# Kernel tuning notes

Measured on AMD Instinct MI355X. Metric: run time of the kernel, lower is better.

Reference implementation:

```python
import jax, jax.numpy as jnp
import numpy as np

S = 4096          # seq_len (longformer-large-4096)
H = 1024          # hidden_size
FF = 3072         # ffnn_size (hardcoded)
G = 100           # number of gold mentions
MAX_SPAN = 30     # max_span_length
TOP_LAMBDA = 0.2
LN_EPS = 1e-5
MASK_VAL = 10000.0


def setup_inputs() -> dict:
    key = jax.random.key(0)
    ks = jax.random.split(key, 16)
    sc = 0.02
    sequence_output = jax.random.normal(ks[0], (1, S, H), jnp.float32)
    attention_mask = jnp.ones((1, S), jnp.int32)
    # valid gold spans: 1 <= start <= end < start + MAX_SPAN (so torch's >0 filter keeps all)
    gs = jax.random.randint(ks[1], (G,), 1, S - MAX_SPAN)
    gl = jax.random.randint(ks[2], (G,), 0, MAX_SPAN)
    gold_mentions = jnp.stack([gs, gs + gl], axis=1).astype(jnp.int32)  # [G, 2]
    inp = {
        'sequence_output': sequence_output,
        'attention_mask': attention_mask,
        'gold_mentions': gold_mentions,
        # start_mention_mlp
        'W_sm': jax.random.normal(ks[3], (H, FF), jnp.float32) * sc,
        'b_sm': jnp.zeros((FF,), jnp.float32),
        'g_sm': jnp.ones((FF,), jnp.float32),
        'beta_sm': jnp.zeros((FF,), jnp.float32),
        # end_mention_mlp
        'W_em': jax.random.normal(ks[4], (H, FF), jnp.float32) * sc,
        'b_em': jnp.zeros((FF,), jnp.float32),
        'g_em': jnp.ones((FF,), jnp.float32),
        'beta_em': jnp.zeros((FF,), jnp.float32),
        # classifiers
        'w_start': jax.random.normal(ks[5], (FF,), jnp.float32) * sc,
        'b_start': jnp.zeros((), jnp.float32),
        'w_end': jax.random.normal(ks[6], (FF,), jnp.float32) * sc,
        'b_end': jnp.zeros((), jnp.float32),
        'W_s2e': jax.random.normal(ks[7], (FF, FF), jnp.float32) * sc,
        'b_s2e': jnp.zeros((FF,), jnp.float32),
    }
    return inp


def _fcl(x, W, b, g, beta):
    # dense -> gelu (exact) -> layernorm (dropout is identity in eval)
    h = jax.nn.gelu(x @ W + b, approximate=False)
    mu = jnp.mean(h, axis=-1, keepdims=True)
    var = jnp.mean(jnp.square(h - mu), axis=-1, keepdims=True)
    return (h - mu) * jax.lax.rsqrt(var + LN_EPS) * g + beta


def _forward(sequence_output, attention_mask, gold_mentions,
             W_sm, b_sm, g_sm, beta_sm, W_em, b_em, g_em, beta_em,
             w_start, b_start, w_end, b_end, W_s2e, b_s2e):
    start_reps = _fcl(sequence_output, W_sm, b_sm, g_sm, beta_sm)  # [1,S,FF]
    end_reps = _fcl(sequence_output, W_em, b_em, g_em, beta_em)    # [1,S,FF]

    start_logits = jnp.einsum('bsf,f->bs', start_reps, w_start) + b_start  # [1,S]
    end_logits = jnp.einsum('bsf,f->bs', end_reps, w_end) + b_end          # [1,S]
    temp = start_reps @ W_s2e + b_s2e                                      # [1,S,FF]
    joint = jnp.einsum('bsf,btf->bst', temp, end_reps)                     # [1,S,S]
    mention_logits = joint + start_logits[:, :, None] + end_logits[:, None, :]

    # span mask: start <= end < start + MAX_SPAN (triu(0) then tril(MAX_SPAN-1))
    i = jnp.arange(S)
    mention_mask = ((i[:, None] <= i[None, :]) & (i[None, :] < i[:, None] + MAX_SPAN)
                    ).astype(jnp.float32)[None]  # [1,S,S]
    mention_logits = jnp.clip(mention_logits + (1.0 - mention_mask) * (-MASK_VAL),
                              -MASK_VAL, MASK_VAL)

    # top-k pruning; attention_mask is full so k is static: int(S * 0.2)
    max_k = int(S * TOP_LAMBDA)  # 819
    _, topk_1d = jax.lax.top_k(mention_logits.reshape(1, -1), max_k)  # [1,max_k]
    sorted_idx = jnp.sort(topk_1d, axis=-1)
    topk_start_ids = sorted_idx // S
    topk_end_ids = sorted_idx % S
    span_mask = jnp.ones((1, max_k), jnp.float32)

    # losses
    probs = jax.nn.sigmoid(mention_logits)  # [1,S,S]
    gstart = gold_mentions[:, 0]
    gend = gold_mentions[:, 1]
    gold_probs = probs[0, gstart, gend]
    # torch BCE clamps log at -100
    cost_gold = -jnp.mean(jnp.maximum(jnp.log(gold_probs), -100.0))
    junk = probs.at[0, gstart, gend].set(0.0)
    log1mp = jnp.maximum(jnp.log(1.0 - junk), -100.0)
    cost_junk = -jnp.sum(jnp.where(mention_mask == 1.0, log1mp, 0.0)) / jnp.sum(mention_mask)
    cost_is_mention = (cost_gold + cost_junk)[None]  # [1]

    return topk_start_ids, topk_end_ids, span_mask, sequence_output, cost_is_mention


def reference(sequence_output, attention_mask, gold_mentions,
              W_sm, b_sm, g_sm, beta_sm, W_em, b_em, g_em, beta_em,
              w_start, b_start, w_end, b_end, W_s2e, b_s2e):
    return _forward(sequence_output, attention_mask, gold_mentions,
                    W_sm, b_sm, g_sm, beta_sm, W_em, b_em, g_em, beta_em,
                    w_start, b_start, w_end, b_end, W_s2e, b_s2e)
```

## Files before the change

### kernel.cpp

```cpp
#include <hip/hip_runtime.h>
#include <math.h>

#define S 4096
#define H 1024
#define FF 3072
#define G 100
#define MAXSPAN 30
#define MAXK 819
#define NBAND (S * MAXSPAN)
#define BAND_COUNT 122445.0

#define O_START 0
#define O_END   819
#define O_MASK  1638
#define O_SEQ   2457
#define O_COST  (2457 + S * H)

typedef __bf16 bf16x8 __attribute__((ext_vector_type(8)));
typedef float f32x4 __attribute__((ext_vector_type(4)));
typedef float f32x16 __attribute__((ext_vector_type(16)));


__device__ __forceinline__ float block_reduce_256(float x, volatile float* red) {
  #pragma unroll
  for (int off = 32; off > 0; off >>= 1) x += __shfl_down(x, off, 64);
  int wid = threadIdx.x >> 6;
  int lane = threadIdx.x & 63;
  __syncthreads();
  if (lane == 0) red[wid] = x;
  __syncthreads();
  return red[0] + red[1] + red[2] + red[3];
}

__device__ __forceinline__ unsigned f2key(float f) {
  unsigned b = __float_as_uint(f);
  return (b & 0x80000000u) ? ~b : (b | 0x80000000u);
}

__device__ __forceinline__ unsigned short bf16_rne(float x) {
  unsigned u = __float_as_uint(x);
  unsigned r = ((u >> 16) & 1u) + 0x7FFFu;
  return (unsigned short)((u + r) >> 16);
}

__device__ __forceinline__ void split2(float x, unsigned short& h, unsigned short& l) {
  h = bf16_rne(x);
  float hf = __uint_as_float(((unsigned)h) << 16);
  l = bf16_rne(x - hf);
}

__device__ __forceinline__ void gld16(const void* g, void* l) {
  __builtin_amdgcn_global_load_lds(
      (const __attribute__((address_space(1))) unsigned int*)g,
      (__attribute__((address_space(3))) unsigned int*)l, 16, 0, 0);
}


__global__ __launch_bounds__(256) void pack_a_kernel(const float* __restrict__ A,
                                                     unsigned short* __restrict__ hi,
                                                     unsigned short* __restrict__ lo,
                                                     int K) {
  __shared__ float tile[32][33];
  const int t = threadIdx.x;
  const int tx = t & 31, ty8 = t >> 5;
  const int k0 = blockIdx.x * 32, r0 = blockIdx.y * 32;
  #pragma unroll
  for (int r = ty8; r < 32; r += 8)
    tile[r][tx] = A[(size_t)(r0 + r) * K + k0 + tx];
  __syncthreads();
  if (t < 128) {
    const int kql = t >> 5;
    const int rl = t & 31;
    unsigned short h8[8], l8[8];
    #pragma unroll
    for (int s = 0; s < 8; s++) split2(tile[rl][kql * 8 + s], h8[s], l8[s]);
    const size_t panel = (size_t)(r0 >> 7);
    const int rloc = (r0 & 127) + rl;
    const size_t off = panel * (size_t)(128 * K) + (size_t)(k0 / 8 + kql) * 1024 + (size_t)rloc * 8;
    *(uint4*)(hi + off) = *(const uint4*)h8;
    *(uint4*)(lo + off) = *(const uint4*)l8;
  }
}

__global__ __launch_bounds__(256) void pack_ln_a_kernel(const float* __restrict__ A,
                                                        const float* __restrict__ mu,
                                                        const float* __restrict__ rstd,
                                                        const float* __restrict__ g,
                                                        const float* __restrict__ beta,
                                                        unsigned short* __restrict__ hi,
                                                        unsigned short* __restrict__ lo,
                                                        int K) {
  __shared__ float tile[32][33];
  const int t = threadIdx.x;
  const int tx = t & 31, ty8 = t >> 5;
  const int k0 = blockIdx.x * 32, r0 = blockIdx.y * 32;
  #pragma unroll
  for (int r = ty8; r < 32; r += 8)
    tile[r][tx] = A[(size_t)(r0 + r) * K + k0 + tx];
  __syncthreads();
  if (t < 128) {
    const int kql = t >> 5;
    const int rl = t & 31;
    const int row = r0 + rl;
    const float m = mu[row], rs = rstd[row];
    float4 g0 = *(const float4*)(g + k0 + kql * 8);
    float4 g1 = *(const float4*)(g + k0 + kql * 8 + 4);
    float4 b0 = *(const float4*)(beta + k0 + kql * 8);
    float4 b1 = *(const float4*)(beta + k0 + kql * 8 + 4);
    float gv[8] = {g0.x, g0.y, g0.z, g0.w, g1.x, g1.y, g1.z, g1.w};
    float bv[8] = {b0.x, b0.y, b0.z, b0.w, b1.x, b1.y, b1.z, b1.w};
    unsigned short h8[8], l8[8];
    #pragma unroll
    for (int s = 0; s < 8; s++) {
      float v = (tile[rl][kql * 8 + s] - m) * rs * gv[s] + bv[s];
      split2(v, h8[s], l8[s]);
    }
    const size_t panel = (size_t)(r0 >> 7);
    const int rloc = (r0 & 127) + rl;
    const size_t off = panel * (size_t)(128 * K) + (size_t)(k0 / 8 + kql) * 1024 + (size_t)rloc * 8;
    *(uint4*)(hi + off) = *(const uint4*)h8;
    *(uint4*)(lo + off) = *(const uint4*)l8;
  }
}

__global__ __launch_bounds__(256) void pack_bt_kernel(const float* __restrict__ W,
                                                      unsigned short* __restrict__ hi,
                                                      unsigned short* __restrict__ lo,
                                                      int K, int N) {
  __shared__ float tile[32][33];
  const int t = threadIdx.x;
  const int tx = t & 31, ty8 = t >> 5;
  const int k0 = blockIdx.x * 32, n0 = blockIdx.y * 32;
  #pragma unroll
  for (int r = ty8; r < 32; r += 8)
    tile[r][tx] = W[(size_t)(k0 + r) * N + n0 + tx];
  __syncthreads();
  if (t < 128) {
    const int kql = t >> 5;
    const int nl = t & 31;
    unsigned short h8[8], l8[8];
    #pragma unroll
    for (int s = 0; s < 8; s++) split2(tile[kql * 8 + s][nl], h8[s], l8[s]);
    const size_t panel = (size_t)(n0 >> 7);
    const int nloc = (n0 & 127) + nl;
    const size_t off = panel * (size_t)(128 * K) + (size_t)(k0 / 8 + kql) * 1024 + (size_t)nloc * 8;
    *(uint4*)(hi + off) = *(const uint4*)h8;
    *(uint4*)(lo + off) = *(const uint4*)l8;
  }
}


template <int EPI>
__device__ __forceinline__ void gemm_body(const char* cAh, const char* cAl,
                                          const char* cBh, const char* cBl,
                                          const float* __restrict__ bias,
                                          float* __restrict__ C,
                                          int bm, int bn, int N, int K,
                                          char* smem) {
  const int tid = threadIdx.x;
  const int lane = tid & 63;
  const int wid = __builtin_amdgcn_readfirstlane(tid >> 6);
  const int wm = wid >> 1, wn = wid & 1;
  const int lb = lane * 16;
  const int ldsq = wid * 2048;

  const int khalf = lane >> 5;
  const int r31 = lane & 31;
  const int abase = khalf * 2048 + (wm * 64 + r31) * 16;
  const int bbase = khalf * 2048 + (wn * 64 + r31) * 16;

  f32x16 acc[2][2];
  #pragma unroll
  for (int a = 0; a < 2; a++)
    #pragma unroll
    for (int b = 0; b < 2; b++)
      #pragma unroll
      for (int r = 0; r < 16; r++) acc[a][b][r] = 0.0f;

  for (int k0 = 0; k0 < K; k0 += 32) {
    const size_t qb = (size_t)((k0 >> 3) + wid) * 2048 + lb;
    __syncthreads();
    gld16(cAh + qb,        smem +     0 + ldsq);
    gld16(cAh + qb + 1024, smem +     0 + ldsq + 1024);
    gld16(cAl + qb,        smem +  8192 + ldsq);
    gld16(cAl + qb + 1024, smem +  8192 + ldsq + 1024);
    gld16(cBh + qb,        smem + 16384 + ldsq);
    gld16(cBh + qb + 1024, smem + 16384 + ldsq + 1024);
    gld16(cBl + qb,        smem + 24576 + ldsq);
    gld16(cBl + qb + 1024, smem + 24576 + ldsq + 1024);
    __syncthreads();

    bf16x8 ah[2][2], al[2][2], bh[2][2], bl[2][2];
    #pragma unroll
    for (int ks = 0; ks < 2; ks++) {
      #pragma unroll
      for (int mt = 0; mt < 2; mt++) {
        ah[ks][mt] = *(const bf16x8*)(smem +     0 + ks * 4096 + abase + mt * 512);
        al[ks][mt] = *(const bf16x8*)(smem +  8192 + ks * 4096 + abase + mt * 512);
      }
      #pragma unroll
      for (int nt = 0; nt < 2; nt++) {
        bh[ks][nt] = *(const bf16x8*)(smem + 16384 + ks * 4096 + bbase + nt * 512);
        bl[ks][nt] = *(const bf16x8*)(smem + 24576 + ks * 4096 + bbase + nt * 512);
      }
    }
    #pragma unroll
    for (int ks = 0; ks < 2; ks++)
      #pragma unroll
      for (int mt = 0; mt < 2; mt++)
        #pragma unroll
        for (int nt = 0; nt < 2; nt++) {
          acc[mt][nt] = __builtin_amdgcn_mfma_f32_32x32x16_bf16(ah[ks][mt], bh[ks][nt], acc[mt][nt], 0, 0, 0);
          acc[mt][nt] = __builtin_amdgcn_mfma_f32_32x32x16_bf16(al[ks][mt], bh[ks][nt], acc[mt][nt], 0, 0, 0);
          acc[mt][nt] = __builtin_amdgcn_mfma_f32_32x32x16_bf16(ah[ks][mt], bl[ks][nt], acc[mt][nt], 0, 0, 0);
        }
  }

  #pragma unroll
  for (int mt = 0; mt < 2; mt++) {
    #pragma unroll
    for (int nt = 0; nt < 2; nt++) {
      const int colg = bn + wn * 64 + nt * 32 + r31;
      const float bb = bias[colg];
      #pragma unroll
      for (int reg = 0; reg < 16; reg++) {
        const int rowl = (reg & 3) + 8 * (reg >> 2) + 4 * khalf;
        const int rowg = bm + wm * 64 + mt * 32 + rowl;
        float v = acc[mt][nt][reg] + bb;
        if (EPI == 1) v = 0.5f * v * (1.0f + erff(v * 0.70710678118654752f));
        C[(size_t)rowg * N + colg] = v;
      }
    }
  }
}

__global__ __launch_bounds__(256) void gemm_mfma_kernel(const unsigned short* __restrict__ Ahi,
                                                        const unsigned short* __restrict__ Alo,
                                                        const unsigned short* __restrict__ Bhi,
                                                        const unsigned short* __restrict__ Blo,
                                                        const float* __restrict__ bias,
                                                        float* __restrict__ C,
                                                        int N, int K) {
  __shared__ __align__(16) char smem[32768];
  const size_t panAb = (size_t)blockIdx.y * (size_t)(128 * K) * 2;
  const size_t panBb = (size_t)blockIdx.x * (size_t)(128 * K) * 2;
  gemm_body<0>((const char*)Ahi + panAb, (const char*)Alo + panAb,
               (const char*)Bhi + panBb, (const char*)Blo + panBb,
               bias, C, blockIdx.y * 128, blockIdx.x * 128, N, K, smem);
}

__global__ __launch_bounds__(256) void gemm_mfma_dual_kernel(const unsigned short* __restrict__ Ahi,
                                                             const unsigned short* __restrict__ Alo,
                                                             const unsigned short* __restrict__ B1hi,
                                                             const unsigned short* __restrict__ B1lo,
                                                             const unsigned short* __restrict__ B2hi,
                                                             const unsigned short* __restrict__ B2lo,
                                                             const float* __restrict__ bias1,
                                                             const float* __restrict__ bias2,
                                                             float* __restrict__ C1,
                                                             float* __restrict__ C2,
                                                             int N, int K) {
  __shared__ __align__(16) char smem[32768];
  const int zb = blockIdx.z;
  const unsigned short* Bhi = zb ? B2hi : B1hi;
  const unsigned short* Blo = zb ? B2lo : B1lo;
  const float* bias = zb ? bias2 : bias1;
  float* C = zb ? C2 : C1;
  const size_t panAb = (size_t)blockIdx.y * (size_t)(128 * K) * 2;
  const size_t panBb = (size_t)blockIdx.x * (size_t)(128 * K) * 2;
  gemm_body<1>((const char*)Ahi + panAb, (const char*)Alo + panAb,
               (const char*)Bhi + panBb, (const char*)Blo + panBb,
               bias, C, blockIdx.y * 128, blockIdx.x * 128, N, K, smem);
}


__global__ __launch_bounds__(256) void ln_stats_kernel(const float* __restrict__ HbS,
                                                       const float* __restrict__ HbE,
                                                       const float* __restrict__ gS,
                                                       const float* __restrict__ betaS,
                                                       const float* __restrict__ wS,
                                                       const float* __restrict__ bS,
                                                       const float* __restrict__ gE,
                                                       const float* __restrict__ betaE,
                                                       const float* __restrict__ wE,
                                                       const float* __restrict__ bE,
                                                       float* __restrict__ slog,
                                                       float* __restrict__ elog,
                                                       float* __restrict__ muS,
                                                       float* __restrict__ rstdS,
                                                       float* __restrict__ muE,
                                                       float* __restrict__ rstdE) {
  __shared__ float red[4];
  const int row = blockIdx.x, tid = threadIdx.x;
  const int br = blockIdx.y;
  const float* Hb = br ? HbE : HbS;
  const float* g = br ? gE : gS;
  const float* beta = br ? betaE : betaS;
  const float* w = br ? wE : wS;
  const float* bsc = br ? bE : bS;
  const float* h = Hb + (size_t)row * FF;

  float4 v[3];
  float s = 0.0f;
  #pragma unroll
  for (int t = 0; t < 3; t++) {
    v[t] = *(const float4*)(h + tid * 4 + t * 1024);
    s += v[t].x + v[t].y + v[t].z + v[t].w;
  }
  float mu = block_reduce_256(s, red) * (1.0f / (float)FF);

  float s2 = 0.0f;
  #pragma unroll
  for (int t = 0; t < 3; t++) {
    float dx = v[t].x - mu, dy = v[t].y - mu, dz = v[t].z - mu, dw = v[t].w - mu;
    s2 += dx * dx + dy * dy + dz * dz + dw * dw;
  }
  float var = block_reduce_256(s2, red) * (1.0f / (float)FF);
  float rstd = rsqrtf(var + 1e-5f);

  float dot = 0.0f;
  #pragma unroll
  for (int t = 0; t < 3; t++) {
    int idx = tid * 4 + t * 1024;
    float4 gv = *(const float4*)(g + idx);
    float4 bv = *(const float4*)(beta + idx);
    float4 wv = *(const float4*)(w + idx);
    float rx = (v[t].x - mu) * rstd * gv.x + bv.x;
    float ry = (v[t].y - mu) * rstd * gv.y + bv.y;
    float rz = (v[t].z - mu) * rstd * gv.z + bv.z;
    float rw = (v[t].w - mu) * rstd * gv.w + bv.w;
    dot += rx * wv.x + ry * wv.y + rz * wv.z + rw * wv.w;
  }
  float dt = block_reduce_256(dot, red);
  if (tid == 0) {
    if (br) { elog[row] = dt + bsc[0]; muE[row] = mu; rstdE[row] = rstd; }
    else    { slog[row] = dt + bsc[0]; muS[row] = mu; rstdS[row] = rstd; }
  }
}


__global__ __launch_bounds__(256) void band_joint_kernel(const float* __restrict__ T,
                                                         const float* __restrict__ Eraw,
                                                         const float* __restrict__ muE,
                                                         const float* __restrict__ rstdE,
                                                         const float* __restrict__ gE,
                                                         const float* __restrict__ betaE,
                                                         const float* __restrict__ sl,
                                                         const float* __restrict__ el,
                                                         float* __restrict__ band) {
  __shared__ float Elds[45][260];
  const int t = threadIdx.x;
  const int bx = blockIdx.x;
  const int sbx = (bx & 7) * 32 + (bx >> 3);
  const int i0 = sbx * 16;
  const int r_l = t >> 4, c = t & 15;

  float accd[MAXSPAN];
  #pragma unroll
  for (int d = 0; d < MAXSPAN; d++) accd[d] = 0.0f;

  for (int k0 = 0; k0 < FF; k0 += 256) {
    const float* trow = T + (size_t)(i0 + r_l) * FF + k0 + c * 16;
    float4 tv0 = *(const float4*)(trow + 0);
    float4 tv1 = *(const float4*)(trow + 4);
    float4 tv2 = *(const float4*)(trow + 8);
    float4 tv3 = *(const float4*)(trow + 12);
    __syncthreads();
    for (int rr = t >> 6; rr < 45; rr += 4) {
      int gr = i0 + rr;
      int cc = (t & 63) * 4;
      float4 rv = {0.f, 0.f, 0.f, 0.f};
      if (gr < S) {
        float4 ev = *(const float4*)(Eraw + (size_t)gr * FF + k0 + cc);
        float m = muE[gr], rs = rstdE[gr];
        float4 gv = *(const float4*)(gE + k0 + cc);
        float4 bv = *(const float4*)(betaE + k0 + cc);
        rv.x = (ev.x - m) * rs * gv.x + bv.x;
        rv.y = (ev.y - m) * rs * gv.y + bv.y;
        rv.z = (ev.z - m) * rs * gv.z + bv.z;
        rv.w = (ev.w - m) * rs * gv.w + bv.w;
      }
      *(float4*)&Elds[rr][cc] = rv;
    }
    __syncthreads();
    #pragma unroll
    for (int d = 0; d < MAXSPAN; d++) {
      const float* er = &Elds[r_l + d][c * 16];
      float4 e0 = *(const float4*)(er + 0);
      float4 e1 = *(const float4*)(er + 4);
      float4 e2 = *(const float4*)(er + 8);
      float4 e3 = *(const float4*)(er + 12);
      accd[d] += tv0.x * e0.x + tv0.y * e0.y + tv0.z * e0.z + tv0.w * e0.w
               + tv1.x * e1.x + tv1.y * e1.y + tv1.z * e1.z + tv1.w * e1.w
               + tv2.x * e2.x + tv2.y * e2.y + tv2.z * e2.z + tv2.w * e2.w
               + tv3.x * e3.x + tv3.y * e3.y + tv3.z * e3.z + tv3.w * e3.w;
    }
  }

  const int i = i0 + r_l;
  const float my_sl = sl[i];
  #pragma unroll
  for (int d = 0; d < MAXSPAN; d++) {
    float v = accd[d];
    v += __shfl_down(v, 8, 16);
    v += __shfl_down(v, 4, 16);
    v += __shfl_down(v, 2, 16);
    v += __shfl_down(v, 1, 16);
    if (c == 0) {
      int j = i + d;
      if (j < S) {
        float vv = v + my_sl + el[j];
        vv = fminf(fmaxf(vv, -10000.0f), 10000.0f);
        band[i * MAXSPAN + d] = vv;
      } else {
        band[i * MAXSPAN + d] = -1e30f;
      }
    }
  }
}


__global__ void mark_gold_kernel(const int* __restrict__ gold, char* __restrict__ mark) {
  int t = threadIdx.x;
  if (t < G) {
    int gs = gold[2 * t], ge = gold[2 * t + 1];
    mark[gs * MAXSPAN + (ge - gs)] = 1;
  }
}

__global__ __launch_bounds__(256) void cost_junk_kernel(const float* __restrict__ band,
                                                        const char* __restrict__ mark,
                                                        double* __restrict__ jacc) {
  __shared__ float red[4];
  int e = blockIdx.x * 256 + threadIdx.x;
  int i = e / MAXSPAN, d = e - i * MAXSPAN;
  float term = 0.0f;
  if (i + d < S && !mark[e]) {
    float x = band[e];
    float p = 1.0f / (1.0f + expf(-x));
    term = fmaxf(logf(1.0f - p), -100.0f);
  }
  float ssum = block_reduce_256(term, red);
  if (threadIdx.x == 0) atomicAdd(jacc, (double)ssum);
}

__global__ __launch_bounds__(256) void finalize_kernel(const float* __restrict__ band,
                                                       const int* __restrict__ gold,
                                                       const double* __restrict__ jacc,
                                                       float* __restrict__ outc) {
  __shared__ float red[4];
  int t = threadIdx.x;
  float term = 0.0f;
  if (t < G) {
    int gs = gold[2 * t], ge = gold[2 * t + 1];
    float x = band[gs * MAXSPAN + (ge - gs)];
    float p = 1.0f / (1.0f + expf(-x));
    term = fmaxf(logf(p), -100.0f);
  }
  float sg = block_reduce_256(term, red);
  if (t == 0) {
    double cost = -((double)sg / (double)G) - ((*jacc) / BAND_COUNT);
    *outc = (float)cost;
  }
}


__global__ __launch_bounds__(1024) void topk_kernel(const float* __restrict__ band,
                                                    float* __restrict__ out) {
  __shared__ int hist[256];
  __shared__ unsigned sh_prefix;
  __shared__ int sh_remk;
  __shared__ int idxbuf[1024];
  __shared__ unsigned tkey[256];
  __shared__ int tidx[256];
  __shared__ int cnt_gt, cnt_eq;
  __shared__ int sb[1024];
  const int tid = threadIdx.x;

  if (tid < 256) hist[tid] = 0;
  __syncthreads();
  for (int e = tid; e < NBAND; e += 1024)
    atomicAdd(&hist[f2key(band[e]) >> 24], 1);
  __syncthreads();
  if (tid == 0) {
    int cum = 0, b = 255;
    for (; b > 0; b--) {
      if (cum + hist[b] >= MAXK) break;
      cum += hist[b];
    }
    sh_prefix = (unsigned)b;
    sh_remk = MAXK - cum;
  }
  __syncthreads();
  const unsigned p8 = sh_prefix;
  int remk = sh_remk;
  __syncthreads();

  if (tid < 256) hist[tid] = 0;
  __syncthreads();
  for (int e = tid; e < NBAND; e += 1024) {
    unsigned key = f2key(band[e]);
    if ((key >> 24) == p8) atomicAdd(&hist[(key >> 16) & 255], 1);
  }
  __syncthreads();
  if (tid == 0) {
    int cum = 0, b = 255;
    for (; b > 0; b--) {
      if (cum + hist[b] >= remk) break;
      cum += hist[b];
    }
    sh_prefix = (p8 << 8) | (unsigned)b;
    sh_remk = remk - cum;
  }
  __syncthreads();
  const unsigned T16 = sh_prefix;
  remk = sh_remk;

  if (tid == 0) { cnt_gt = 0; cnt_eq = 0; }
  __syncthreads();
  for (int e = tid; e < NBAND; e += 1024) {
    unsigned key = f2key(band[e]);
    unsigned k16 = key >> 16;
    if (k16 >= T16) {
      int i = e / MAXSPAN, d = e - i * MAXSPAN;
      int fi = i * S + i + d;
      if (k16 > T16) {
        int p = atomicAdd(&cnt_gt, 1);
        if (p < 1024) idxbuf[p] = fi;
      } else {
        int p = atomicAdd(&cnt_eq, 1);
        if (p < 256) { tkey[p] = key; tidx[p] = fi; }
      }
    }
  }
  __syncthreads();
  if (tid == 0) {
    int ngt = cnt_gt < 1024 ? cnt_gt : 1024;
    int ne = cnt_eq < 256 ? cnt_eq : 256;
    for (int a2 = 1; a2 < ne; a2++) {
      unsigned kv = tkey[a2]; int iv = tidx[a2];
      int b2 = a2 - 1;
      while (b2 >= 0 && (tkey[b2] < kv || (tkey[b2] == kv && tidx[b2] > iv))) {
        tkey[b2 + 1] = tkey[b2]; tidx[b2 + 1] = tidx[b2]; b2--;
      }
      tkey[b2 + 1] = kv; tidx[b2 + 1] = iv;
    }
    int take = remk < ne ? remk : ne;
    for (int q = 0; q < take; q++)
      if (ngt + q < 1024) idxbuf[ngt + q] = tidx[q];
  }
  __syncthreads();

  sb[tid] = (tid < MAXK) ? idxbuf[tid] : 0x7FFFFFFF;
  __syncthreads();
  for (int ksz = 2; ksz <= 1024; ksz <<= 1) {
    for (int jj = ksz >> 1; jj > 0; jj >>= 1) {
      int ixj = tid ^ jj;
      if (ixj > tid) {
        int a2 = sb[tid], b2 = sb[ixj];
        bool up = ((tid & ksz) == 0);
        if (up ? (a2 > b2) : (a2 < b2)) { sb[tid] = b2; sb[ixj] = a2; }
      }
      __syncthreads();
    }
  }
  if (tid < MAXK) {
    int fi = sb[tid];
    out[O_START + tid] = (float)(fi >> 12);
    out[O_END + tid]   = (float)(fi & 4095);
    out[O_MASK + tid]  = 1.0f;
  }
}


extern "C" void kernel_launch(void* const* d_in, const int* in_sizes, int n_in,
                              void* d_out, int out_size, void* d_ws, size_t ws_size,
                              hipStream_t stream) {
  (void)in_sizes; (void)n_in; (void)out_size; (void)ws_size;
  const float* seq    = (const float*)d_in[0];
  const int*   gold   = (const int*)d_in[2];
  const float* W_sm   = (const float*)d_in[3];
  const float* b_sm   = (const float*)d_in[4];
  const float* g_sm   = (const float*)d_in[5];
  const float* be_sm  = (const float*)d_in[6];
  const float* W_em   = (const float*)d_in[7];
  const float* b_em   = (const float*)d_in[8];
  const float* g_em   = (const float*)d_in[9];
  const float* be_em  = (const float*)d_in[10];
  const float* w_st   = (const float*)d_in[11];
  const float* b_st   = (const float*)d_in[12];
  const float* w_en   = (const float*)d_in[13];
  const float* b_en   = (const float*)d_in[14];
  const float* W_s2e  = (const float*)d_in[15];
  const float* b_s2e  = (const float*)d_in[16];
  float* out = (float*)d_out;
  char* ws = (char*)d_ws;

  const size_t SZ_REP = (size_t)S * FF * 4;
  float*  bufS = (float*)(ws);
  float*  bufE = (float*)(ws + SZ_REP);
  float*  bufT = (float*)(ws + 2 * SZ_REP);
  char* R3 = ws + 3 * SZ_REP;
  unsigned short* seqhi = (unsigned short*)R3;
  unsigned short* seqlo = (unsigned short*)(R3 + (size_t)S * H * 2);
  unsigned short* a3hi  = (unsigned short*)R3;
  unsigned short* a3lo  = (unsigned short*)(R3 + (size_t)S * FF * 2);
  char* R4 = ws + 4 * SZ_REP;
  const size_t SZ_W12 = (size_t)H * FF * 2;
  unsigned short* wb1hi = (unsigned short*)R4;
  unsigned short* wb1lo = (unsigned short*)(R4 + SZ_W12);
  unsigned short* wb2hi = (unsigned short*)(R4 + 2 * SZ_W12);
  unsigned short* wb2lo = (unsigned short*)(R4 + 3 * SZ_W12);
  unsigned short* wbhi = (unsigned short*)R4;
  unsigned short* wblo = (unsigned short*)(R4 + (size_t)FF * FF * 2);
  char* R5 = R4 + 2 * (size_t)FF * FF * 2;
  float*  band = (float*)R5;
  char*   mark = R5 + (size_t)NBAND * 4;
  double* jacc = (double*)(R5 + (size_t)NBAND * 4 + NBAND + 32);
  float*  slog = (float*)(R5 + (size_t)NBAND * 4 + NBAND + 128);
  float*  elog  = slog + S;
  float*  muS   = elog + S;
  float*  rstdS = muS + S;
  float*  muE   = rstdS + S;
  float*  rstdE = muE + S;

  hipMemsetAsync(mark, 0, NBAND, stream);
  hipMemsetAsync(jacc, 0, 8, stream);

  dim3 gg(FF / 128, S / 128);
  dim3 gg2(FF / 128, S / 128, 2);

  pack_a_kernel<<<dim3(H / 32, S / 32), 256, 0, stream>>>(seq, seqhi, seqlo, H);
  pack_bt_kernel<<<dim3(H / 32, FF / 32), 256, 0, stream>>>(W_sm, wb1hi, wb1lo, H, FF);
  pack_bt_kernel<<<dim3(H / 32, FF / 32), 256, 0, stream>>>(W_em, wb2hi, wb2lo, H, FF);
  gemm_mfma_dual_kernel<<<gg2, 256, 0, stream>>>(seqhi, seqlo, wb1hi, wb1lo, wb2hi, wb2lo,
                                                 b_sm, b_em, bufS, bufE, FF, H);
  ln_stats_kernel<<<dim3(S, 2), 256, 0, stream>>>(bufS, bufE, g_sm, be_sm, w_st, b_st,
                                                  g_em, be_em, w_en, b_en,
                                                  slog, elog, muS, rstdS, muE, rstdE);
  pack_ln_a_kernel<<<dim3(FF / 32, S / 32), 256, 0, stream>>>(bufS, muS, rstdS, g_sm, be_sm, a3hi, a3lo, FF);
  pack_bt_kernel<<<dim3(FF / 32, FF / 32), 256, 0, stream>>>(W_s2e, wbhi, wblo, FF, FF);
  gemm_mfma_kernel<<<gg, 256, 0, stream>>>(a3hi, a3lo, wbhi, wblo, b_s2e, bufT, FF, FF);

  band_joint_kernel<<<S / 16, 256, 0, stream>>>(bufT, bufE, muE, rstdE, g_em, be_em,
                                                slog, elog, band);

  mark_gold_kernel<<<1, 128, 0, stream>>>(gold, mark);
  cost_junk_kernel<<<NBAND / 256, 256, 0, stream>>>(band, mark, jacc);
  topk_kernel<<<1, 1024, 0, stream>>>(band, out);
  finalize_kernel<<<1, 256, 0, stream>>>(band, gold, jacc, out + O_COST);

  hipMemcpyAsync(out + O_SEQ, seq, (size_t)S * H * 4, hipMemcpyDeviceToDevice, stream);
}
```

Measured before the change: 824.3 us.

## Double-buffer GEMM LDS staging and fuse junk-cost, gold, topk and pack kernels

The GEMM k-loop now uses two 32KB LDS buffers and prefetches the next k-slab before computing the current one, dropping one barrier per iteration. This is meant to overlap global loads with MFMA work, at the cost of doubling shared memory per block, which may lower occupancy. Separately, the junk log-loss sum moves into the band kernel, and the gold correction (with dedup) folds into the topk kernel, removing the mark buffer, its memset and three launches. The two weight pack kernels also merge into one z-indexed launch.

```diff
diff --git a/kernel.cpp b/kernel.cpp
--- a/kernel.cpp
+++ b/kernel.cpp
@@ -17,7 +17,6 @@
 #define O_COST  (2457 + S * H)
 
 typedef __bf16 bf16x8 __attribute__((ext_vector_type(8)));
-typedef float f32x4 __attribute__((ext_vector_type(4)));
 typedef float f32x16 __attribute__((ext_vector_type(16)));
 
 
@@ -30,6 +29,20 @@
   if (lane == 0) red[wid] = x;
   __syncthreads();
   return red[0] + red[1] + red[2] + red[3];
+}
+
+__device__ __forceinline__ float block_reduce_1024(float x, volatile float* red) {
+  #pragma unroll
+  for (int off = 32; off > 0; off >>= 1) x += __shfl_down(x, off, 64);
+  int wid = threadIdx.x >> 6;
+  int lane = threadIdx.x & 63;
+  __syncthreads();
+  if (lane == 0) red[wid] = x;
+  __syncthreads();
+  float s = 0.f;
+  #pragma unroll
+  for (int q = 0; q < 16; q++) s += red[q];
+  return s;
 }
 
 __device__ __forceinline__ unsigned f2key(float f) {
@@ -123,10 +136,10 @@
   }
 }
 
-__global__ __launch_bounds__(256) void pack_bt_kernel(const float* __restrict__ W,
-                                                      unsigned short* __restrict__ hi,
-                                                      unsigned short* __restrict__ lo,
-                                                      int K, int N) {
+__device__ __forceinline__ void pack_bt_body(const float* __restrict__ W,
+                                             unsigned short* __restrict__ hi,
+                                             unsigned short* __restrict__ lo,
+                                             int K, int N) {
   __shared__ float tile[32][33];
   const int t = threadIdx.x;
   const int tx = t & 31, ty8 = t >> 5;
@@ -147,6 +160,24 @@
     *(uint4*)(hi + off) = *(const uint4*)h8;
     *(uint4*)(lo + off) = *(const uint4*)l8;
   }
+}
+
+__global__ __launch_bounds__(256) void pack_bt_kernel(const float* __restrict__ W,
+                                                      unsigned short* __restrict__ hi,
+                                                      unsigned short* __restrict__ lo,
+                                                      int K, int N) {
+  pack_bt_body(W, hi, lo, K, N);
+}
+
+__global__ __launch_bounds__(256) void pack_bt_dual_kernel(const float* __restrict__ W1,
+                                                           const float* __restrict__ W2,
+                                                           unsigned short* __restrict__ h1,
+                                                           unsigned short* __restrict__ l1,
+                                                           unsigned short* __restrict__ h2,
+                                                           unsigned short* __restrict__ l2,
+                                                           int K, int N) {
+  if (blockIdx.z == 0) pack_bt_body(W1, h1, l1, K, N);
+  else                 pack_bt_body(W2, h2, l2, K, N);
 }
 
 
@@ -177,31 +208,38 @@
       #pragma unroll
       for (int r = 0; r < 16; r++) acc[a][b][r] = 0.0f;
 
+  auto stage = [&](int buf, int k0) {
+    const size_t qb = (size_t)((k0 >> 3) + wid) * 2048 + lb;
+    char* sbuf = smem + buf * 32768 + ldsq;
+    gld16(cAh + qb,        sbuf +     0);
+    gld16(cAh + qb + 1024, sbuf +     0 + 1024);
+    gld16(cAl + qb,        sbuf +  8192);
+    gld16(cAl + qb + 1024, sbuf +  8192 + 1024);
+    gld16(cBh + qb,        sbuf + 16384);
+    gld16(cBh + qb + 1024, sbuf + 16384 + 1024);
+    gld16(cBl + qb,        sbuf + 24576);
+    gld16(cBl + qb + 1024, sbuf + 24576 + 1024);
+  };
+
+  stage(0, 0);
   for (int k0 = 0; k0 < K; k0 += 32) {
-    const size_t qb = (size_t)((k0 >> 3) + wid) * 2048 + lb;
+    const int cur = (k0 >> 5) & 1;
     __syncthreads();
-    gld16(cAh + qb,        smem +     0 + ldsq);
-    gld16(cAh + qb + 1024, smem +     0 + ldsq + 1024);
-    gld16(cAl + qb,        smem +  8192 + ldsq);
-    gld16(cAl + qb + 1024, smem +  8192 + ldsq + 1024);
-    gld16(cBh + qb,        smem + 16384 + ldsq);
-    gld16(cBh + qb + 1024, smem + 16384 + ldsq + 1024);
-    gld16(cBl + qb,        smem + 24576 + ldsq);
-    gld16(cBl + qb + 1024, smem + 24576 + ldsq + 1024);
-    __syncthreads();
+    if (k0 + 32 < K) stage(cur ^ 1, k0 + 32);
+    const char* sm = smem + cur * 32768;
 
     bf16x8 ah[2][2], al[2][2], bh[2][2], bl[2][2];
     #pragma unroll
     for (int ks = 0; ks < 2; ks++) {
       #pragma unroll
       for (int mt = 0; mt < 2; mt++) {
-        ah[ks][mt] = *(const bf16x8*)(smem +     0 + ks * 4096 + abase + mt * 512);
-        al[ks][mt] = *(const bf16x8*)(smem +  8192 + ks * 4096 + abase + mt * 512);
+        ah[ks][mt] = *(const bf16x8*)(sm +     0 + ks * 4096 + abase + mt * 512);
+        al[ks][mt] = *(const bf16x8*)(sm +  8192 + ks * 4096 + abase + mt * 512);
       }
       #pragma unroll
       for (int nt = 0; nt < 2; nt++) {
-        bh[ks][nt] = *(const bf16x8*)(smem + 16384 + ks * 4096 + bbase + nt * 512);
-        bl[ks][nt] = *(const bf16x8*)(smem + 24576 + ks * 4096 + bbase + nt * 512);
+        bh[ks][nt] = *(const bf16x8*)(sm + 16384 + ks * 4096 + bbase + nt * 512);
+        bl[ks][nt] = *(const bf16x8*)(sm + 24576 + ks * 4096 + bbase + nt * 512);
       }
     }
     #pragma unroll
@@ -241,7 +279,7 @@
                                                         const float* __restrict__ bias,
                                                         float* __restrict__ C,
                                                         int N, int K) {
-  __shared__ __align__(16) char smem[32768];
+  __shared__ __align__(16) char smem[65536];
   const size_t panAb = (size_t)blockIdx.y * (size_t)(128 * K) * 2;
   const size_t panBb = (size_t)blockIdx.x * (size_t)(128 * K) * 2;
   gemm_body<0>((const char*)Ahi + panAb, (const char*)Alo + panAb,
@@ -260,7 +298,7 @@
                                                              float* __restrict__ C1,
                                                              float* __restrict__ C2,
                                                              int N, int K) {
-  __shared__ __align__(16) char smem[32768];
+  __shared__ __align__(16) char smem[65536];
   const int zb = blockIdx.z;
   const unsigned short* Bhi = zb ? B2hi : B1hi;
   const unsigned short* Blo = zb ? B2lo : B1lo;
@@ -347,8 +385,10 @@
                                                          const float* __restrict__ betaE,
                                                          const float* __restrict__ sl,
                                                          const float* __restrict__ el,
-                                                         float* __restrict__ band) {
+                                                         float* __restrict__ band,
+                                                         double* __restrict__ jacc) {
   __shared__ float Elds[45][260];
+  __shared__ float red[4];
   const int t = threadIdx.x;
   const int bx = blockIdx.x;
   const int sbx = (bx & 7) * 32 + (bx >> 3);
@@ -399,6 +439,7 @@
 
   const int i = i0 + r_l;
   const float my_sl = sl[i];
+  float jsum = 0.0f;
   #pragma unroll
   for (int d = 0; d < MAXSPAN; d++) {
     float v = accd[d];
@@ -412,61 +453,22 @@
         float vv = v + my_sl + el[j];
         vv = fminf(fmaxf(vv, -10000.0f), 10000.0f);
         band[i * MAXSPAN + d] = vv;
+        float p = 1.0f / (1.0f + expf(-vv));
+        jsum += fmaxf(logf(1.0f - p), -100.0f);
       } else {
         band[i * MAXSPAN + d] = -1e30f;
       }
     }
   }
-}
-
-
-__global__ void mark_gold_kernel(const int* __restrict__ gold, char* __restrict__ mark) {
-  int t = threadIdx.x;
-  if (t < G) {
-    int gs = gold[2 * t], ge = gold[2 * t + 1];
-    mark[gs * MAXSPAN + (ge - gs)] = 1;
-  }
-}
-
-__global__ __launch_bounds__(256) void cost_junk_kernel(const float* __restrict__ band,
-                                                        const char* __restrict__ mark,
-                                                        double* __restrict__ jacc) {
-  __shared__ float red[4];
-  int e = blockIdx.x * 256 + threadIdx.x;
-  int i = e / MAXSPAN, d = e - i * MAXSPAN;
-  float term = 0.0f;
-  if (i + d < S && !mark[e]) {
-    float x = band[e];
-    float p = 1.0f / (1.0f + expf(-x));
-    term = fmaxf(logf(1.0f - p), -100.0f);
-  }
-  float ssum = block_reduce_256(term, red);
-  if (threadIdx.x == 0) atomicAdd(jacc, (double)ssum);
-}
-
-__global__ __launch_bounds__(256) void finalize_kernel(const float* __restrict__ band,
-                                                       const int* __restrict__ gold,
-                                                       const double* __restrict__ jacc,
-                                                       float* __restrict__ outc) {
-  __shared__ float red[4];
-  int t = threadIdx.x;
-  float term = 0.0f;
-  if (t < G) {
-    int gs = gold[2 * t], ge = gold[2 * t + 1];
-    float x = band[gs * MAXSPAN + (ge - gs)];
-    float p = 1.0f / (1.0f + expf(-x));
-    term = fmaxf(logf(p), -100.0f);
-  }
-  float sg = block_reduce_256(term, red);
-  if (t == 0) {
-    double cost = -((double)sg / (double)G) - ((*jacc) / BAND_COUNT);
-    *outc = (float)cost;
-  }
-}
-
-
-__global__ __launch_bounds__(1024) void topk_kernel(const float* __restrict__ band,
-                                                    float* __restrict__ out) {
+  float tot = block_reduce_256(jsum, red);
+  if (t == 0) atomicAdd(jacc, (double)tot);
+}
+
+
+__global__ __launch_bounds__(1024) void topk_finalize_kernel(const float* __restrict__ band,
+                                                             const int* __restrict__ gold,
+                                                             const double* __restrict__ jacc,
+                                                             float* __restrict__ out) {
   __shared__ int hist[256];
   __shared__ unsigned sh_prefix;
   __shared__ int sh_remk;
@@ -475,6 +477,8 @@
   __shared__ int tidx[256];
   __shared__ int cnt_gt, cnt_eq;
   __shared__ int sb[1024];
+  __shared__ int gcell[G];
+  __shared__ float redf[16];
   const int tid = threadIdx.x;
 
   if (tid < 256) hist[tid] = 0;
@@ -569,6 +573,30 @@
     out[O_START + tid] = (float)(fi >> 12);
     out[O_END + tid]   = (float)(fi & 4095);
     out[O_MASK + tid]  = 1.0f;
+  }
+
+  if (tid < G) {
+    int gs = gold[2 * tid], ge = gold[2 * tid + 1];
+    gcell[tid] = gs * MAXSPAN + (ge - gs);
+  }
+  __syncthreads();
+  float tg = 0.0f, tj = 0.0f;
+  if (tid < G) {
+    int cell = gcell[tid];
+    float x = band[cell];
+    float p = 1.0f / (1.0f + expf(-x));
+    tg = fmaxf(logf(p), -100.0f);
+    bool first = true;
+    for (int q = 0; q < tid; q++)
+      if (gcell[q] == cell) { first = false; break; }
+    if (first) tj = fmaxf(logf(1.0f - p), -100.0f);
+  }
+  float sg = block_reduce_1024(tg, redf);
+  float sj = block_reduce_1024(tj, redf);
+  if (tid == 0) {
+    double junk = *jacc - (double)sj;
+    double cost = -((double)sg / (double)G) - (junk / BAND_COUNT);
+    out[O_COST] = (float)cost;
   }
 }
 
@@ -615,24 +643,22 @@
   unsigned short* wblo = (unsigned short*)(R4 + (size_t)FF * FF * 2);
   char* R5 = R4 + 2 * (size_t)FF * FF * 2;
   float*  band = (float*)R5;
-  char*   mark = R5 + (size_t)NBAND * 4;
-  double* jacc = (double*)(R5 + (size_t)NBAND * 4 + NBAND + 32);
-  float*  slog = (float*)(R5 + (size_t)NBAND * 4 + NBAND + 128);
+  double* jacc = (double*)(R5 + (size_t)NBAND * 4);
+  float*  slog = (float*)(R5 + (size_t)NBAND * 4 + 64);
   float*  elog  = slog + S;
   float*  muS   = elog + S;
   float*  rstdS = muS + S;
   float*  muE   = rstdS + S;
   float*  rstdE = muE + S;
 
-  hipMemsetAsync(mark, 0, NBAND, stream);
   hipMemsetAsync(jacc, 0, 8, stream);
 
   dim3 gg(FF / 128, S / 128);
   dim3 gg2(FF / 128, S / 128, 2);
 
   pack_a_kernel<<<dim3(H / 32, S / 32), 256, 0, stream>>>(seq, seqhi, seqlo, H);
-  pack_bt_kernel<<<dim3(H / 32, FF / 32), 256, 0, stream>>>(W_sm, wb1hi, wb1lo, H, FF);
-  pack_bt_kernel<<<dim3(H / 32, FF / 32), 256, 0, stream>>>(W_em, wb2hi, wb2lo, H, FF);
+  pack_bt_dual_kernel<<<dim3(H / 32, FF / 32, 2), 256, 0, stream>>>(W_sm, W_em,
+                                                                    wb1hi, wb1lo, wb2hi, wb2lo, H, FF);
   gemm_mfma_dual_kernel<<<gg2, 256, 0, stream>>>(seqhi, seqlo, wb1hi, wb1lo, wb2hi, wb2lo,
                                                  b_sm, b_em, bufS, bufE, FF, H);
   ln_stats_kernel<<<dim3(S, 2), 256, 0, stream>>>(bufS, bufE, g_sm, be_sm, w_st, b_st,
@@ -643,12 +669,9 @@
   gemm_mfma_kernel<<<gg, 256, 0, stream>>>(a3hi, a3lo, wbhi, wblo, b_s2e, bufT, FF, FF);
 
   band_joint_kernel<<<S / 16, 256, 0, stream>>>(bufT, bufE, muE, rstdE, g_em, be_em,
-                                                slog, elog, band);
-
-  mark_gold_kernel<<<1, 128, 0, stream>>>(gold, mark);
-  cost_junk_kernel<<<NBAND / 256, 256, 0, stream>>>(band, mark, jacc);
-  topk_kernel<<<1, 1024, 0, stream>>>(band, out);
-  finalize_kernel<<<1, 256, 0, stream>>>(band, gold, jacc, out + O_COST);
+                                                slog, elog, band, jacc);
+
+  topk_finalize_kernel<<<1, 1024, 0, stream>>>(band, gold, jacc, out);
 
   hipMemcpyAsync(out + O_SEQ, seq, (size_t)S * H * 4, hipMemcpyDeviceToDevice, stream);
 }
```

New measurement: 824.2 us. About the same (-0.0%).
